# Performance work log

Hardware: AMD Instinct MI355X
Metric: run time of the kernel (lower is better)

Reference implementation:

```python
import jax, jax.numpy as jnp
import numpy as np

K = 5        # kernel_size per dim
DIM = 3      # pseudo-coordinate dim
KTOT = K ** DIM   # 125 kernel weight matrices
S = 2 ** DIM      # 8 basis products for degree-1 open B-spline
KNN = 3


def spline_basis(ea):
    """Degree-1 open B-spline basis. ea: [E, DIM] in [0,1).
    Returns basis [E, S] and kernel weight indices wi [E, S]."""
    v = ea * (K - 1)
    b = jnp.floor(v)
    f = v - b                      # fractional part, grads flow here
    bi = b.astype(jnp.int32)
    bases, idxs = [], []
    for c in range(S):             # static loop over 2^DIM corner combos
        bs = jnp.ones(ea.shape[0], ea.dtype)
        wi = jnp.zeros(ea.shape[0], jnp.int32)
        for d in range(DIM):
            bit = (c >> d) & 1
            bs = bs * (f[:, d] if bit else 1.0 - f[:, d])
            wi = wi + jnp.clip(bi[:, d] + bit, 0, K - 1) * (K ** d)
        bases.append(bs)
        idxs.append(wi)
    return jnp.stack(bases, 1), jnp.stack(idxs, 1)


def spline_conv(x, src, dst, basis, wi, W, Wroot, bias):
    """SplineConv with aggr='mean', root weight and bias (PyG defaults)."""
    N, Cin = x.shape
    E = src.shape[0]
    xs = x[src]                                   # [E, Cin] gather
    vals = xs[:, None, :] * basis[:, :, None]     # [E, S, Cin]
    seg = (dst[:, None] * KTOT + wi).reshape(-1)  # bucket by (dst node, kernel)
    A = jax.ops.segment_sum(vals.reshape(-1, Cin), seg,
                            num_segments=N * KTOT).reshape(N, KTOT, Cin)
    out = jnp.einsum('nki,kio->no', A, W)         # apply kernel bank once
    deg = jax.ops.segment_sum(jnp.ones(E, x.dtype), dst, num_segments=N)
    out = out / jnp.maximum(deg, 1.0)[:, None]    # mean aggregation
    return out + x @ Wroot + bias


def knn_interpolate(x, pos_x, pos_y, batch_x, batch_y, k):
    """PyG knn_interpolate: inverse-squared-distance weighted k-NN average."""
    off = 1e5  # separate batches in coordinate space
    px = pos_x + batch_x[:, None].astype(pos_x.dtype) * off
    py = pos_y + batch_y[:, None].astype(pos_y.dtype) * off
    d2 = (jnp.sum(py ** 2, 1)[:, None] + jnp.sum(px ** 2, 1)[None, :]
          - 2.0 * (py @ px.T))                    # [Ny, Nx]
    negd, idx = jax.lax.top_k(-d2, k)             # k nearest
    w = 1.0 / jnp.maximum(-negd, 1e-16)           # [Ny, k]
    return (w[:, :, None] * x[idx]).sum(1) / w.sum(1)[:, None]


def setup_inputs() -> dict:
    key = jax.random.key(0)
    ks = jax.random.split(key, 12)
    N, E, Ny, C = 8192, 131072, 16384, 64
    return {
        'x': jax.random.normal(ks[0], (N, C), jnp.float32),
        'edge_index': jax.random.randint(ks[1], (2, E), 0, N, jnp.int32),
        'edge_attr': jax.random.uniform(ks[2], (E, DIM), jnp.float32),
        'pos_x': jax.random.normal(ks[3], (N, 3), jnp.float32),
        'batch_x': jnp.zeros((N,), jnp.int32),
        'pos_y': jax.random.normal(ks[4], (Ny, 3), jnp.float32),
        'batch_y': jnp.zeros((Ny,), jnp.int32),
        'Wa': jax.random.normal(ks[5], (KTOT, C, C), jnp.float32) * 0.05,
        'roota': jax.random.normal(ks[6], (C, C), jnp.float32) * 0.05,
        'biasa': jnp.zeros((C,), jnp.float32),
        'Wb': jax.random.normal(ks[7], (KTOT, C, C), jnp.float32) * 0.05,
        'rootb': jax.random.normal(ks[8], (C, C), jnp.float32) * 0.05,
        'biasb': jnp.zeros((C,), jnp.float32),
    }


def reference(x, edge_index, edge_attr, pos_x, batch_x, pos_y, batch_y,
              Wa, roota, biasa, Wb, rootb, biasb):
    src, dst = edge_index[0], edge_index[1]
    basis, wi = spline_basis(edge_attr)
    h = jax.nn.elu(spline_conv(x, src, dst, basis, wi, Wa, roota, biasa))
    h = jax.nn.elu(spline_conv(h, src, dst, basis, wi, Wb, rootb, biasb))
    return knn_interpolate(h, pos_x, pos_y, batch_x, batch_y, KNN)
```

## Files before the change

kernel.cpp:

```cpp
#include <hip/hip_runtime.h>
#include <hip/hip_bf16.h>
#include <math.h>

#define CDIV(a,b) (((a)+(b)-1)/(b))
#define WPCV 8
#define KCH 32

typedef __attribute__((ext_vector_type(8))) short bf16x8;
typedef __attribute__((ext_vector_type(4))) float f32x4;

__device__ __forceinline__ float elu_f(float x){ return x > 0.f ? x : expm1f(x); }
__device__ __forceinline__ unsigned short f2bf(float x){
    __hip_bfloat16 h = __float2bfloat16(x);
    union { __hip_bfloat16 b; unsigned short u; } cv; cv.b = h; return cv.u;
}
__device__ __forceinline__ float bf2f(unsigned short u){
    unsigned int ui = ((unsigned int)u) << 16;
    union { unsigned int u; float f; } cv; cv.u = ui; return cv.f;
}

__global__ void k_basis(const float* __restrict__ ea, const int* __restrict__ dst,
                        float* __restrict__ basis, int* __restrict__ cellid,
                        int* __restrict__ cellcnt, int* __restrict__ deg,
                        int* __restrict__ rank, int E)
{
    __shared__ int hist[64];
    const int tid = threadIdx.x;
    if (tid < 64) hist[tid] = 0;
    __syncthreads();
    int e = blockIdx.x * blockDim.x + tid;
    if (e < E) {
        float f[3]; int bi[3];
        #pragma unroll
        for (int d = 0; d < 3; d++) {
            float v = ea[e*3+d] * 4.f;
            float b = floorf(v);
            f[d] = v - b;
            int bb = (int)b; bb = bb < 0 ? 0 : (bb > 3 ? 3 : bb);
            bi[d] = bb;
        }
        int cell = bi[0] + 4*bi[1] + 16*bi[2];
        cellid[e] = cell;
        atomicAdd(&hist[cell], 1);
        rank[e] = atomicAdd(deg + dst[e], 1);
        float bs[8];
        #pragma unroll
        for (int c = 0; c < 8; c++) {
            float b = 1.f;
            #pragma unroll
            for (int d = 0; d < 3; d++)
                b *= ((c>>d)&1) ? f[d] : (1.f - f[d]);
            bs[c] = b;
        }
        float4* bw = (float4*)(basis + (size_t)e*8);
        bw[0] = make_float4(bs[0],bs[1],bs[2],bs[3]);
        bw[1] = make_float4(bs[4],bs[5],bs[6],bs[7]);
    }
    __syncthreads();
    if (tid < 64 && hist[tid]) atomicAdd(cellcnt + tid, hist[tid]);
}

__global__ void k_scan(const int* __restrict__ cnt, int* __restrict__ start, int* __restrict__ fill)
{
    if (threadIdx.x == 0 && blockIdx.x == 0) {
        int s = 0;
        for (int i = 0; i < 64; i++) { start[i] = s; fill[i] = s; s += cnt[i]; }
        start[64] = s;
    }
}

__global__ void k_scatter(const int* __restrict__ cellid, int* __restrict__ fill,
                          int* __restrict__ elist, int E)
{
    __shared__ int hist[64], bas[64];
    const int tid = threadIdx.x;
    if (tid < 64) hist[tid] = 0;
    __syncthreads();
    int e = blockIdx.x * blockDim.x + tid;
    int cell = 0, loc = 0;
    bool act = e < E;
    if (act) { cell = cellid[e]; loc = atomicAdd(&hist[cell], 1); }
    __syncthreads();
    if (tid < 64) bas[tid] = hist[tid] ? atomicAdd(fill + tid, hist[tid]) : 0;
    __syncthreads();
    if (act) elist[bas[cell] + loc] = e;
}

__global__ __launch_bounds__(1024) void k_degscan(const int* __restrict__ deg,
                        int* __restrict__ csr, float* __restrict__ invdeg, int N)
{
    __shared__ int buf[2][1024];
    const int t = threadIdx.x;
    const int base = t*8;
    int loc[8]; int s = 0;
    #pragma unroll
    for (int j = 0; j < 8; j++) {
        loc[j] = s;
        int d = (base+j < N) ? deg[base+j] : 0;
        if (base+j < N) invdeg[base+j] = 1.f / fmaxf((float)d, 1.f);
        s += d;
    }
    buf[0][t] = s; __syncthreads();
    int pb = 0;
    for (int off = 1; off < 1024; off <<= 1) {
        int v = buf[pb][t];
        if (t >= off) v += buf[pb][t-off];
        buf[pb^1][t] = v; __syncthreads(); pb ^= 1;
    }
    int excl = buf[pb][t] - s;
    #pragma unroll
    for (int j = 0; j < 8; j++)
        if (base+j < N) csr[base+j] = excl + loc[j];
    if (t == 0) csr[N] = buf[pb][1023];
}

__global__ void k_eord(const int* __restrict__ dst, const int* __restrict__ rank,
                       const int* __restrict__ csr, int* __restrict__ eord, int E)
{
    int e = blockIdx.x * blockDim.x + threadIdx.x;
    if (e < E) eord[csr[dst[e]] + rank[e]] = e;
}

__global__ void k_wprep(const float* __restrict__ Wa, const float* __restrict__ Wb,
                        unsigned short* __restrict__ WTa, unsigned short* __restrict__ WTb)
{
    __shared__ float ws[64][65];
    const int b = blockIdx.x;
    const float* Wsrc = (b < 125) ? (Wa + (size_t)b*4096) : (Wb + (size_t)(b-125)*4096);
    unsigned short* Wdst = (b < 125) ? (WTa + (size_t)b*4096) : (WTb + (size_t)(b-125)*4096);
    const int tid = threadIdx.x;
    #pragma unroll
    for (int j = 0; j < 16; j++) {
        int idx = j*256 + tid;
        ws[idx>>6][idx&63] = Wsrc[idx];
    }
    __syncthreads();
    #pragma unroll
    for (int j = 0; j < 16; j++) {
        int idx = j*256 + tid;
        int o = idx>>6, i = idx&63;
        Wdst[idx] = f2bf(ws[i][o]);
    }
}

__global__ __launch_bounds__(256) void k_conv(
    const float* __restrict__ xin, const unsigned short* __restrict__ WT,
    const int* __restrict__ elist, const int* __restrict__ cellstart,
    const float* __restrict__ basis, const int* __restrict__ src,
    unsigned short* __restrict__ ye)
{
    __shared__ unsigned short wt[8][64][64];
    __shared__ unsigned short xb[64][64];
    __shared__ float bts[8][64];
    __shared__ int eids[64];

    const int cell = blockIdx.x / WPCV;
    const int sub  = blockIdx.x % WPCV;
    const int tid  = threadIdx.x;
    const int w    = tid >> 6;
    const int lane = tid & 63;
    const int eh   = w >> 1;
    const int oh   = w & 1;
    const int l15  = lane & 15;
    const int kgrp = lane >> 4;
    const int swz  = lane & 7;

    int kc[8];
    {
        int b0 = cell & 3, b1 = (cell >> 2) & 3, b2 = (cell >> 4) & 3;
        #pragma unroll
        for (int c = 0; c < 8; c++)
            kc[c] = (b0 + (c&1)) + 5*(b1 + ((c>>1)&1)) + 25*(b2 + ((c>>2)&1));
    }

    #pragma unroll
    for (int j = 0; j < 16; j++) {
        int cj  = j >> 1;
        int off = ((j & 1) << 8) + tid;
        int row = off >> 3, colc = off & 7;
        bf16x8 v = ((const bf16x8*)(WT + (size_t)kc[cj]*4096))[off];
        *(bf16x8*)&wt[cj][row][(colc ^ (row & 7)) << 3] = v;
    }

    const int s0 = cellstart[cell], s1 = cellstart[cell+1];
    const int se = tid >> 2, sm = tid & 3;

    for (int base = s0 + sub*64; base < s1; base += WPCV*64) {
        int ne = s1 - base; ne = ne > 64 ? 64 : ne;
        __syncthreads();
        if (se < ne) {
            int eid = elist[base + se];
            int sn  = src[eid];
            const float4* xr = (const float4*)(xin + (size_t)sn*64);
            unsigned short tmp[16];
            #pragma unroll
            for (int j = 0; j < 4; j++) {
                float4 v = xr[sm*4 + j];
                tmp[j*4+0] = f2bf(v.x); tmp[j*4+1] = f2bf(v.y);
                tmp[j*4+2] = f2bf(v.z); tmp[j*4+3] = f2bf(v.w);
            }
            int c0 = (sm*2)     ^ (se & 7);
            int c1 = (sm*2 + 1) ^ (se & 7);
            *(bf16x8*)&xb[se][c0 << 3] = *(bf16x8*)&tmp[0];
            *(bf16x8*)&xb[se][c1 << 3] = *(bf16x8*)&tmp[8];
            if (sm == 0) {
                const float4* br = (const float4*)(basis + (size_t)eid*8);
                float4 bA = br[0], bB = br[1];
                bts[0][se]=bA.x; bts[1][se]=bA.y; bts[2][se]=bA.z; bts[3][se]=bA.w;
                bts[4][se]=bB.x; bts[5][se]=bB.y; bts[6][se]=bB.z; bts[7][se]=bB.w;
                eids[se] = eid;
            }
        } else if (sm == 0) {
            eids[se] = -1;
        }
        __syncthreads();

        bf16x8 a[2][2];
        #pragma unroll
        for (int me = 0; me < 2; me++) {
            int arow = eh*32 + me*16 + l15;
            #pragma unroll
            for (int kh = 0; kh < 2; kh++)
                a[me][kh] = *(const bf16x8*)&xb[arow][((kh*4 + kgrp) ^ swz) << 3];
        }

        f32x4 y[2][2] = {{{0,0,0,0},{0,0,0,0}},{{0,0,0,0},{0,0,0,0}}};
        #pragma unroll
        for (int c = 0; c < 8; c++) {
            float4 bv[2];
            bv[0] = *(const float4*)&bts[c][eh*32 +      (kgrp << 2)];
            bv[1] = *(const float4*)&bts[c][eh*32 + 16 + (kgrp << 2)];
            bf16x8 bfr[2][2];
            #pragma unroll
            for (int nb = 0; nb < 2; nb++) {
                int brow = oh*32 + nb*16 + l15;
                #pragma unroll
                for (int kh = 0; kh < 2; kh++)
                    bfr[nb][kh] = *(const bf16x8*)&wt[c][brow][((kh*4 + kgrp) ^ swz) << 3];
            }
            #pragma unroll
            for (int me = 0; me < 2; me++) {
                #pragma unroll
                for (int nb = 0; nb < 2; nb++) {
                    f32x4 t = {0.f, 0.f, 0.f, 0.f};
                    t = __builtin_amdgcn_mfma_f32_16x16x32_bf16(a[me][0], bfr[nb][0], t, 0, 0, 0);
                    t = __builtin_amdgcn_mfma_f32_16x16x32_bf16(a[me][1], bfr[nb][1], t, 0, 0, 0);
                    y[me][nb][0] = fmaf(bv[me].x, t[0], y[me][nb][0]);
                    y[me][nb][1] = fmaf(bv[me].y, t[1], y[me][nb][1]);
                    y[me][nb][2] = fmaf(bv[me].z, t[2], y[me][nb][2]);
                    y[me][nb][3] = fmaf(bv[me].w, t[3], y[me][nb][3]);
                }
            }
        }
        #pragma unroll
        for (int me = 0; me < 2; me++) {
            #pragma unroll
            for (int r = 0; r < 4; r++) {
                int el  = eh*32 + me*16 + (kgrp << 2) + r;
                int eid = eids[el];
                if (eid >= 0) {
                    unsigned short* yp = ye + (size_t)eid*64 + oh*32 + l15;
                    yp[0]  = f2bf(y[me][0][r]);
                    yp[16] = f2bf(y[me][1][r]);
                }
            }
        }
    }
}

__global__ __launch_bounds__(256) void k_gather(
    const unsigned short* __restrict__ ye, const int* __restrict__ eord,
    const int* __restrict__ csr, const float* __restrict__ xin,
    const float* __restrict__ root, const float* __restrict__ bias,
    const float* __restrict__ invdeg, float* __restrict__ hout, int N)
{
    const int w = threadIdx.x >> 6, lane = threadIdx.x & 63;
    const int n = blockIdx.x*4 + w;
    if (n >= N) return;
    const int s0 = csr[n], s1 = csr[n+1];
    float acc0 = 0.f, acc1 = 0.f;
    int j = s0;
    for (; j + 1 < s1; j += 2) {
        int e0 = eord[j], e1 = eord[j+1];
        acc0 += bf2f(ye[(size_t)e0*64 + lane]);
        acc1 += bf2f(ye[(size_t)e1*64 + lane]);
    }
    if (j < s1) acc0 += bf2f(ye[(size_t)eord[j]*64 + lane]);
    float acc = (acc0 + acc1) * invdeg[n];
    float xv = xin[(size_t)n*64 + lane];
    float rt = bias[lane];
    #pragma unroll 8
    for (int i = 0; i < 64; i++)
        rt = fmaf(__shfl(xv, i, 64), root[i*64 + lane], rt);
    hout[(size_t)n*64 + lane] = elu_f(acc + rt);
}

__global__ void k_px(const float* __restrict__ posx, const int* __restrict__ bx,
                     float4* __restrict__ px4, int N)
{
    int n = blockIdx.x * blockDim.x + threadIdx.x;
    if (n >= N) return;
    float off = (float)bx[n] * 1e5f;
    float a = posx[n*3+0]+off, b = posx[n*3+1]+off, c = posx[n*3+2]+off;
    px4[n] = make_float4(a, b, c, a*a + b*b + c*c);
}

__global__ __launch_bounds__(256) void k_knn_part(
    const float4* __restrict__ px4, const float* __restrict__ posy,
    const int* __restrict__ by, float* __restrict__ pd, int* __restrict__ pi,
    int N, int Ny)
{
    const int qb  = (blockIdx.x / KCH) * 256;
    const int ch  = blockIdx.x % KCH;
    const int NC  = N / KCH;
    const int tid = threadIdx.x;
    const int q = qb + tid;
    float off = (float)by[q] * 1e5f;
    float qa = posy[q*3+0]+off, qbv = posy[q*3+1]+off, qc = posy[q*3+2]+off;
    float sy = qa*qa + qbv*qbv + qc*qc;
    float qa2 = -2.f*qa, qb2 = -2.f*qbv, qc2 = -2.f*qc;

    const float4* __restrict__ pts = px4 + (size_t)ch * NC;
    const int gbase = ch * NC;

    float d0 = 3.4e38f, d1 = 3.4e38f, d2s = 3.4e38f;
    int   i0 = 0x7fffffff, i1 = 0x7fffffff, i2 = 0x7fffffff;
    #pragma unroll 8
    for (int p = 0; p < NC; p++) {
        float4 pt = pts[p];
        float s  = sy + pt.w;
        float u  = fmaf(qa2, pt.x, fmaf(qb2, pt.y, fmaf(qc2, pt.z, s)));
        int   gi = gbase + p;
        bool c0 = u < d0;
        float Md = c0 ? d0 : u;  int Mi = c0 ? i0 : gi;
        d0 = c0 ? u : d0;        i0 = c0 ? gi : i0;
        bool c1 = Md < d1;
        float Md1 = c1 ? d1 : Md; int Mi1 = c1 ? i1 : Mi;
        d1 = c1 ? Md : d1;        i1 = c1 ? Mi : i1;
        bool c2 = Md1 < d2s;
        d2s = c2 ? Md1 : d2s;     i2 = c2 ? Mi1 : i2;
    }
    size_t ob = ((size_t)q*KCH + ch)*3;
    pd[ob+0]=d0; pd[ob+1]=d1; pd[ob+2]=d2s;
    pi[ob+0]=i0; pi[ob+1]=i1; pi[ob+2]=i2;
}

__global__ __launch_bounds__(256) void k_knn_merge(
    const float* __restrict__ pd, const int* __restrict__ pi,
    const float* __restrict__ h2, float* __restrict__ out, int Ny)
{
    const int w = threadIdx.x >> 6, lane = threadIdx.x & 63;
    const int q = blockIdx.x*4 + w;
    const float* pdq = pd + (size_t)q*(KCH*3);
    const int*   piq = pi + (size_t)q*(KCH*3);
    float a0 = pdq[lane];
    int   a0i = piq[lane];
    float a1 = 3.4e38f; int a1i = 0x7fffffff;
    if (lane < KCH*3 - 64) { a1 = pdq[64 + lane]; a1i = piq[64 + lane]; }
    float rd[3]; int ri[3];
    #pragma unroll
    for (int j = 0; j < 3; j++) {
        bool c = (a1 < a0) || (a1 == a0 && a1i < a0i);
        float md = c ? a1 : a0; int mi = c ? a1i : a0i;
        #pragma unroll
        for (int s = 1; s < 64; s <<= 1) {
            float od = __shfl_xor(md, s, 64);
            int   oi = __shfl_xor(mi, s, 64);
            if (od < md || (od == md && oi < mi)) { md = od; mi = oi; }
        }
        rd[j] = md; ri[j] = mi;
        if (a0i == mi) { a0 = 3.4e38f; a0i = 0x7fffffff; }
        if (a1i == mi) { a1 = 3.4e38f; a1i = 0x7fffffff; }
    }
    float w0 = 1.f/fmaxf(rd[0], 1e-16f);
    float w1 = 1.f/fmaxf(rd[1], 1e-16f);
    float w2 = 1.f/fmaxf(rd[2], 1e-16f);
    float ws = w0 + w1 + w2;
    float v = w0*h2[(size_t)ri[0]*64+lane] + w1*h2[(size_t)ri[1]*64+lane]
            + w2*h2[(size_t)ri[2]*64+lane];
    out[(size_t)q*64+lane] = v / ws;
}

extern "C" void kernel_launch(void* const* d_in, const int* in_sizes, int n_in,
                              void* d_out, int out_size, void* d_ws, size_t ws_size,
                              hipStream_t stream)
{
    const float* x     = (const float*)d_in[0];
    const int*   ei    = (const int*)d_in[1];
    const float* ea    = (const float*)d_in[2];
    const float* posx  = (const float*)d_in[3];
    const int*   bx    = (const int*)d_in[4];
    const float* posy  = (const float*)d_in[5];
    const int*   by    = (const int*)d_in[6];
    const float* Wa    = (const float*)d_in[7];
    const float* roota = (const float*)d_in[8];
    const float* biasa = (const float*)d_in[9];
    const float* Wb    = (const float*)d_in[10];
    const float* rootb = (const float*)d_in[11];
    const float* biasb = (const float*)d_in[12];

    const int N  = in_sizes[0] / 64;
    const int E  = in_sizes[1] / 2;
    const int Ny = in_sizes[5] / 3;
    const int* srcp = ei;
    const int* dstp = ei + E;

    char* ws = (char*)d_ws;
    size_t off = 0;
    auto alloc = [&](size_t bytes) { void* p = ws + off; off += (bytes + 255) & ~255ull; return p; };
    float*  basis    = (float*)alloc((size_t)E*8*4);
    int*    cellid   = (int*)  alloc((size_t)E*4);
    int*    rank     = (int*)  alloc((size_t)E*4);
    int*    elist    = (int*)  alloc((size_t)E*4);
    int*    eord     = (int*)  alloc((size_t)E*4);
    int*    deg      = (int*)  alloc((size_t)N*4);
    int*    csr      = (int*)  alloc((size_t)(N+1)*4);
    float*  invdeg   = (float*)alloc((size_t)N*4);
    int*    cellcnt  = (int*)  alloc(64*4);
    int*    cellstart= (int*)  alloc(65*4);
    int*    cellfill = (int*)  alloc(64*4);
    float*  h1       = (float*)alloc((size_t)N*64*4);
    float*  h2       = (float*)alloc((size_t)N*64*4);
    float4* px4      = (float4*)alloc((size_t)N*16);
    unsigned short* WTa = (unsigned short*)alloc((size_t)125*4096*2);
    unsigned short* WTb = (unsigned short*)alloc((size_t)125*4096*2);
    unsigned short* ye  = (unsigned short*)alloc((size_t)E*64*2);
    float* pd = (float*)ye;
    int*   pi = (int*)((char*)ye + ((size_t)8<<20));
    (void)ws_size; (void)n_in; (void)out_size;

    hipMemsetAsync(deg, 0, (size_t)N*4, stream);
    hipMemsetAsync(cellcnt, 0, 64*4, stream);

    k_basis  <<<CDIV(E,256), 256, 0, stream>>>(ea, dstp, basis, cellid, cellcnt, deg, rank, E);
    k_scan   <<<1, 64, 0, stream>>>(cellcnt, cellstart, cellfill);
    k_scatter<<<CDIV(E,256), 256, 0, stream>>>(cellid, cellfill, elist, E);
    k_degscan<<<1, 1024, 0, stream>>>(deg, csr, invdeg, N);
    k_eord   <<<CDIV(E,256), 256, 0, stream>>>(dstp, rank, csr, eord, E);
    k_wprep  <<<250, 256, 0, stream>>>(Wa, Wb, WTa, WTb);
    k_px     <<<CDIV(N,256), 256, 0, stream>>>(posx, bx, px4, N);

    k_conv  <<<64*WPCV, 256, 0, stream>>>(x, WTa, elist, cellstart, basis, srcp, ye);
    k_gather<<<CDIV(N,4), 256, 0, stream>>>(ye, eord, csr, x, roota, biasa, invdeg, h1, N);

    k_conv  <<<64*WPCV, 256, 0, stream>>>(h1, WTb, elist, cellstart, basis, srcp, ye);
    k_gather<<<CDIV(N,4), 256, 0, stream>>>(ye, eord, csr, h1, rootb, biasb, invdeg, h2, N);

    k_knn_part <<<(Ny/256)*KCH, 256, 0, stream>>>(px4, posy, by, pd, pi, N, Ny);
    k_knn_merge<<<Ny/4, 256, 0, stream>>>(pd, pi, h2, (float*)d_out, Ny);
}
```

Before: 202.8 us.

## Merge preprocessing kernels and streamline kNN top-3 selection and merge

Fuses basis/px, the cell scan into the degree scan, and scatter/eord/weight-prep into a single block-partitioned pack kernel, cutting launches from seven plus two memsets to three plus one memset. The kNN partial kernel uses fmed3/fmin-based top-3 insertion, 512-thread blocks, deeper unrolling, and a chunk-major output layout. The merge kernel reads only per-chunk sorted triples and pops from the head instead of doing a two-slot search. The new block sizes and merge logic assume Ny is divisible by 512 and that cellcnt sits directly after deg so one memset clears both.

```diff
diff --git a/kernel.cpp b/kernel.cpp
--- a/kernel.cpp
+++ b/kernel.cpp
@@ -19,13 +19,24 @@
     union { unsigned int u; float f; } cv; cv.u = ui; return cv.f;
 }
 
-__global__ void k_basis(const float* __restrict__ ea, const int* __restrict__ dst,
+__global__ void k_basis_px(const float* __restrict__ ea, const int* __restrict__ dst,
                         float* __restrict__ basis, int* __restrict__ cellid,
                         int* __restrict__ cellcnt, int* __restrict__ deg,
-                        int* __restrict__ rank, int E)
-{
+                        int* __restrict__ rank, int E, int EB,
+                        const float* __restrict__ posx, const int* __restrict__ bx,
+                        float4* __restrict__ px4, int N)
+{
+    const int tid = threadIdx.x;
+    if ((int)blockIdx.x >= EB) {
+        int n = ((int)blockIdx.x - EB)*256 + tid;
+        if (n < N) {
+            float off = (float)bx[n] * 1e5f;
+            float a = posx[n*3+0]+off, b = posx[n*3+1]+off, c = posx[n*3+2]+off;
+            px4[n] = make_float4(a, b, c, a*a + b*b + c*c);
+        }
+        return;
+    }
     __shared__ int hist[64];
-    const int tid = threadIdx.x;
     if (tid < 64) hist[tid] = 0;
     __syncthreads();
     int e = blockIdx.x * blockDim.x + tid;
@@ -60,37 +71,24 @@
     if (tid < 64 && hist[tid]) atomicAdd(cellcnt + tid, hist[tid]);
 }
 
-__global__ void k_scan(const int* __restrict__ cnt, int* __restrict__ start, int* __restrict__ fill)
-{
-    if (threadIdx.x == 0 && blockIdx.x == 0) {
-        int s = 0;
-        for (int i = 0; i < 64; i++) { start[i] = s; fill[i] = s; s += cnt[i]; }
-        start[64] = s;
-    }
-}
-
-__global__ void k_scatter(const int* __restrict__ cellid, int* __restrict__ fill,
-                          int* __restrict__ elist, int E)
-{
-    __shared__ int hist[64], bas[64];
-    const int tid = threadIdx.x;
-    if (tid < 64) hist[tid] = 0;
-    __syncthreads();
-    int e = blockIdx.x * blockDim.x + tid;
-    int cell = 0, loc = 0;
-    bool act = e < E;
-    if (act) { cell = cellid[e]; loc = atomicAdd(&hist[cell], 1); }
-    __syncthreads();
-    if (tid < 64) bas[tid] = hist[tid] ? atomicAdd(fill + tid, hist[tid]) : 0;
-    __syncthreads();
-    if (act) elist[bas[cell] + loc] = e;
-}
-
 __global__ __launch_bounds__(1024) void k_degscan(const int* __restrict__ deg,
-                        int* __restrict__ csr, float* __restrict__ invdeg, int N)
+                        int* __restrict__ csr, float* __restrict__ invdeg, int N,
+                        const int* __restrict__ cellcnt, int* __restrict__ cellstart,
+                        int* __restrict__ cellfill)
 {
     __shared__ int buf[2][1024];
     const int t = threadIdx.x;
+    if (t < 64) {
+        int v = cellcnt[t];
+        int s = v;
+        #pragma unroll
+        for (int off = 1; off < 64; off <<= 1) {
+            int o = __shfl_up(s, off, 64);
+            if (t >= off) s += o;
+        }
+        cellstart[t] = s - v; cellfill[t] = s - v;
+        if (t == 63) cellstart[64] = s;
+    }
     const int base = t*8;
     int loc[8]; int s = 0;
     #pragma unroll
@@ -114,32 +112,49 @@
     if (t == 0) csr[N] = buf[pb][1023];
 }
 
-__global__ void k_eord(const int* __restrict__ dst, const int* __restrict__ rank,
-                       const int* __restrict__ csr, int* __restrict__ eord, int E)
-{
-    int e = blockIdx.x * blockDim.x + threadIdx.x;
-    if (e < E) eord[csr[dst[e]] + rank[e]] = e;
-}
-
-__global__ void k_wprep(const float* __restrict__ Wa, const float* __restrict__ Wb,
-                        unsigned short* __restrict__ WTa, unsigned short* __restrict__ WTb)
-{
-    __shared__ float ws[64][65];
-    const int b = blockIdx.x;
-    const float* Wsrc = (b < 125) ? (Wa + (size_t)b*4096) : (Wb + (size_t)(b-125)*4096);
-    unsigned short* Wdst = (b < 125) ? (WTa + (size_t)b*4096) : (WTb + (size_t)(b-125)*4096);
+__global__ __launch_bounds__(256) void k_pack(
+    const int* __restrict__ cellid, int* __restrict__ fill, int* __restrict__ elist,
+    const int* __restrict__ dst, const int* __restrict__ rank,
+    const int* __restrict__ csr, int* __restrict__ eord, int E, int SB,
+    const float* __restrict__ Wa, const float* __restrict__ Wb,
+    unsigned short* __restrict__ WTa, unsigned short* __restrict__ WTb)
+{
+    __shared__ float shbuf[64*65];
     const int tid = threadIdx.x;
-    #pragma unroll
-    for (int j = 0; j < 16; j++) {
-        int idx = j*256 + tid;
-        ws[idx>>6][idx&63] = Wsrc[idx];
-    }
-    __syncthreads();
-    #pragma unroll
-    for (int j = 0; j < 16; j++) {
-        int idx = j*256 + tid;
-        int o = idx>>6, i = idx&63;
-        Wdst[idx] = f2bf(ws[i][o]);
+    const int bid = blockIdx.x;
+    if (bid < SB) {
+        int* hist = (int*)shbuf;
+        int* bas  = hist + 64;
+        if (tid < 64) hist[tid] = 0;
+        __syncthreads();
+        int e = bid * 256 + tid;
+        int cell = 0, loc = 0;
+        bool act = e < E;
+        if (act) { cell = cellid[e]; loc = atomicAdd(&hist[cell], 1); }
+        __syncthreads();
+        if (tid < 64) bas[tid] = hist[tid] ? atomicAdd(fill + tid, hist[tid]) : 0;
+        __syncthreads();
+        if (act) elist[bas[cell] + loc] = e;
+    } else if (bid < 2*SB) {
+        int e = (bid - SB) * 256 + tid;
+        if (e < E) eord[csr[dst[e]] + rank[e]] = e;
+    } else {
+        int b = bid - 2*SB;
+        float (*ws65)[65] = (float(*)[65])shbuf;
+        const float* Wsrc = (b < 125) ? (Wa + (size_t)b*4096) : (Wb + (size_t)(b-125)*4096);
+        unsigned short* Wdst = (b < 125) ? (WTa + (size_t)b*4096) : (WTb + (size_t)(b-125)*4096);
+        #pragma unroll
+        for (int j = 0; j < 16; j++) {
+            int idx = j*256 + tid;
+            ws65[idx>>6][idx&63] = Wsrc[idx];
+        }
+        __syncthreads();
+        #pragma unroll
+        for (int j = 0; j < 16; j++) {
+            int idx = j*256 + tid;
+            int o = idx>>6, i = idx&63;
+            Wdst[idx] = f2bf(ws65[i][o]);
+        }
     }
 }
 
@@ -295,22 +310,12 @@
     hout[(size_t)n*64 + lane] = elu_f(acc + rt);
 }
 
-__global__ void k_px(const float* __restrict__ posx, const int* __restrict__ bx,
-                     float4* __restrict__ px4, int N)
-{
-    int n = blockIdx.x * blockDim.x + threadIdx.x;
-    if (n >= N) return;
-    float off = (float)bx[n] * 1e5f;
-    float a = posx[n*3+0]+off, b = posx[n*3+1]+off, c = posx[n*3+2]+off;
-    px4[n] = make_float4(a, b, c, a*a + b*b + c*c);
-}
-
-__global__ __launch_bounds__(256) void k_knn_part(
+__global__ __launch_bounds__(512) void k_knn_part(
     const float4* __restrict__ px4, const float* __restrict__ posy,
     const int* __restrict__ by, float* __restrict__ pd, int* __restrict__ pi,
     int N, int Ny)
 {
-    const int qb  = (blockIdx.x / KCH) * 256;
+    const int qb  = (blockIdx.x / KCH) * 512;
     const int ch  = blockIdx.x % KCH;
     const int NC  = N / KCH;
     const int tid = threadIdx.x;
@@ -325,22 +330,21 @@
 
     float d0 = 3.4e38f, d1 = 3.4e38f, d2s = 3.4e38f;
     int   i0 = 0x7fffffff, i1 = 0x7fffffff, i2 = 0x7fffffff;
-    #pragma unroll 8
+    #pragma unroll 16
     for (int p = 0; p < NC; p++) {
         float4 pt = pts[p];
-        float s  = sy + pt.w;
-        float u  = fmaf(qa2, pt.x, fmaf(qb2, pt.y, fmaf(qc2, pt.z, s)));
+        float u  = fmaf(qa2, pt.x, fmaf(qb2, pt.y, fmaf(qc2, pt.z, sy + pt.w)));
         int   gi = gbase + p;
-        bool c0 = u < d0;
-        float Md = c0 ? d0 : u;  int Mi = c0 ? i0 : gi;
-        d0 = c0 ? u : d0;        i0 = c0 ? gi : i0;
-        bool c1 = Md < d1;
-        float Md1 = c1 ? d1 : Md; int Mi1 = c1 ? i1 : Mi;
-        d1 = c1 ? Md : d1;        i1 = c1 ? Mi : i1;
-        bool c2 = Md1 < d2s;
-        d2s = c2 ? Md1 : d2s;     i2 = c2 ? Mi1 : i2;
-    }
-    size_t ob = ((size_t)q*KCH + ch)*3;
+        bool c0 = u < d0, c1 = u < d1, c2 = u < d2s;
+        float nd0 = fminf(d0, u);
+        float nd1 = __builtin_amdgcn_fmed3f(d0, u, d1);
+        float nd2 = __builtin_amdgcn_fmed3f(u, d1, d2s);
+        i2 = c1 ? i1 : (c2 ? gi : i2);
+        i1 = c0 ? i0 : (c1 ? gi : i1);
+        i0 = c0 ? gi : i0;
+        d0 = nd0; d1 = nd1; d2s = nd2;
+    }
+    size_t ob = ((size_t)ch*Ny + q)*3;
     pd[ob+0]=d0; pd[ob+1]=d1; pd[ob+2]=d2s;
     pi[ob+0]=i0; pi[ob+1]=i1; pi[ob+2]=i2;
 }
@@ -351,17 +355,17 @@
 {
     const int w = threadIdx.x >> 6, lane = threadIdx.x & 63;
     const int q = blockIdx.x*4 + w;
-    const float* pdq = pd + (size_t)q*(KCH*3);
-    const int*   piq = pi + (size_t)q*(KCH*3);
-    float a0 = pdq[lane];
-    int   a0i = piq[lane];
-    float a1 = 3.4e38f; int a1i = 0x7fffffff;
-    if (lane < KCH*3 - 64) { a1 = pdq[64 + lane]; a1i = piq[64 + lane]; }
+    float a0 = 3.4e38f, a1 = 3.4e38f, a2 = 3.4e38f;
+    int   b0 = 0x7fffffff, b1 = 0x7fffffff, b2 = 0x7fffffff;
+    if (lane < KCH) {
+        size_t base = ((size_t)lane*Ny + q)*3;
+        a0 = pd[base+0]; a1 = pd[base+1]; a2 = pd[base+2];
+        b0 = pi[base+0]; b1 = pi[base+1]; b2 = pi[base+2];
+    }
     float rd[3]; int ri[3];
     #pragma unroll
     for (int j = 0; j < 3; j++) {
-        bool c = (a1 < a0) || (a1 == a0 && a1i < a0i);
-        float md = c ? a1 : a0; int mi = c ? a1i : a0i;
+        float md = a0; int mi = b0;
         #pragma unroll
         for (int s = 1; s < 64; s <<= 1) {
             float od = __shfl_xor(md, s, 64);
@@ -369,8 +373,7 @@
             if (od < md || (od == md && oi < mi)) { md = od; mi = oi; }
         }
         rd[j] = md; ri[j] = mi;
-        if (a0i == mi) { a0 = 3.4e38f; a0i = 0x7fffffff; }
-        if (a1i == mi) { a1 = 3.4e38f; a1i = 0x7fffffff; }
+        if (b0 == mi) { a0=a1; b0=b1; a1=a2; b1=b2; a2=3.4e38f; b2=0x7fffffff; }
     }
     float w0 = 1.f/fmaxf(rd[0], 1e-16f);
     float w1 = 1.f/fmaxf(rd[1], 1e-16f);
@@ -414,9 +417,9 @@
     int*    elist    = (int*)  alloc((size_t)E*4);
     int*    eord     = (int*)  alloc((size_t)E*4);
     int*    deg      = (int*)  alloc((size_t)N*4);
+    int*    cellcnt  = (int*)  alloc(64*4);
     int*    csr      = (int*)  alloc((size_t)(N+1)*4);
     float*  invdeg   = (float*)alloc((size_t)N*4);
-    int*    cellcnt  = (int*)  alloc(64*4);
     int*    cellstart= (int*)  alloc(65*4);
     int*    cellfill = (int*)  alloc(64*4);
     float*  h1       = (float*)alloc((size_t)N*64*4);
@@ -429,16 +432,16 @@
     int*   pi = (int*)((char*)ye + ((size_t)8<<20));
     (void)ws_size; (void)n_in; (void)out_size;
 
-    hipMemsetAsync(deg, 0, (size_t)N*4, stream);
-    hipMemsetAsync(cellcnt, 0, 64*4, stream);
-
-    k_basis  <<<CDIV(E,256), 256, 0, stream>>>(ea, dstp, basis, cellid, cellcnt, deg, rank, E);
-    k_scan   <<<1, 64, 0, stream>>>(cellcnt, cellstart, cellfill);
-    k_scatter<<<CDIV(E,256), 256, 0, stream>>>(cellid, cellfill, elist, E);
-    k_degscan<<<1, 1024, 0, stream>>>(deg, csr, invdeg, N);
-    k_eord   <<<CDIV(E,256), 256, 0, stream>>>(dstp, rank, csr, eord, E);
-    k_wprep  <<<250, 256, 0, stream>>>(Wa, Wb, WTa, WTb);
-    k_px     <<<CDIV(N,256), 256, 0, stream>>>(posx, bx, px4, N);
+    const int EB = CDIV(E,256);
+    const int PB = CDIV(N,256);
+
+    hipMemsetAsync(deg, 0, (size_t)N*4 + 256, stream);
+
+    k_basis_px<<<EB+PB, 256, 0, stream>>>(ea, dstp, basis, cellid, cellcnt, deg, rank,
+                                          E, EB, posx, bx, px4, N);
+    k_degscan <<<1, 1024, 0, stream>>>(deg, csr, invdeg, N, cellcnt, cellstart, cellfill);
+    k_pack    <<<2*EB + 250, 256, 0, stream>>>(cellid, cellfill, elist, dstp, rank,
+                                               csr, eord, E, EB, Wa, Wb, WTa, WTb);
 
     k_conv  <<<64*WPCV, 256, 0, stream>>>(x, WTa, elist, cellstart, basis, srcp, ye);
     k_gather<<<CDIV(N,4), 256, 0, stream>>>(ye, eord, csr, x, roota, biasa, invdeg, h1, N);
@@ -446,6 +449,6 @@
     k_conv  <<<64*WPCV, 256, 0, stream>>>(h1, WTb, elist, cellstart, basis, srcp, ye);
     k_gather<<<CDIV(N,4), 256, 0, stream>>>(ye, eord, csr, h1, rootb, biasb, invdeg, h2, N);
 
-    k_knn_part <<<(Ny/256)*KCH, 256, 0, stream>>>(px4, posy, by, pd, pi, N, Ny);
+    k_knn_part <<<(Ny/512)*KCH, 512, 0, stream>>>(px4, posy, by, pd, pi, N, Ny);
     k_knn_merge<<<Ny/4, 256, 0, stream>>>(pd, pi, h2, (float*)d_out, Ny);
 }
```

New measurement: 182.5 us. 1.11x faster.
